# Kernel optimization log

Measured on AMD Instinct MI355X. Metric: run time of the kernel, lower is better.

Reference implementation:

```python
import jax, jax.numpy as jnp
import numpy as np

LEAKY_SLOPE = 0.25
EPS_COS = 1e-8
EPS_NORM = 1e-12


def cosine_dist(x):
    # 1 - cosine similarity, matching cosine_distance_torch
    w = jnp.linalg.norm(x, axis=1, keepdims=True)  # [n,1]
    return 1.0 - (x @ x.T) / jnp.maximum(w * w.T, EPS_COS)


def gen_adj(x, edge_per_node):
    # gen_tr_adj_mat: threshold = (edge_per_node*n)-th smallest pairwise cosine distance,
    # zero diagonal, symmetrize via elementwise max, add I, L1 row-normalize.
    n = x.shape[0]
    dist = cosine_dist(x)  # [n,n]
    k = edge_per_node * n
    param = jax.lax.stop_gradient(jnp.partition(dist.ravel(), k)[k])
    eye = jnp.eye(n, dtype=x.dtype)
    g = (dist <= param).astype(x.dtype) * (1.0 - eye)
    adj = (1.0 - dist) * g
    adj_t = adj.T
    take_t = (adj_t > adj).astype(x.dtype)
    adj = adj + adj_t * take_t - adj * take_t  # elementwise max-symmetrize
    adj = adj + eye
    row_norm = jnp.maximum(jnp.sum(jnp.abs(adj), axis=1, keepdims=True), EPS_NORM)
    return adj / row_norm


def gcn_layer(x, adj, w, b):
    # dense mm -> (sparse) adj mm -> bias -> leaky_relu
    return jax.nn.leaky_relu(adj @ (x @ w) + b, LEAKY_SLOPE)


def setup_inputs() -> dict:
    key = jax.random.key(0)
    ks = jax.random.split(key, 8)
    n, d = 4000, 1000
    h = [400, 400, 200]
    x = jax.random.normal(ks[0], (n, d), jnp.float32)

    def xavier(k, fi, fo):
        std = (2.0 / (fi + fo)) ** 0.5
        return std * jax.random.normal(k, (fi, fo), jnp.float32)

    w1 = xavier(ks[1], d, h[0])
    w2 = xavier(ks[2], h[0], h[1])
    w3 = xavier(ks[3], h[1], h[2])
    b1 = jnp.zeros((h[0],), jnp.float32)
    b2 = jnp.zeros((h[1],), jnp.float32)
    b3 = jnp.zeros((h[2],), jnp.float32)
    adj_parameter = 10
    adj = gen_adj(x, adj_parameter)  # initial train adjacency, as in the pipeline
    return dict(adj_parameter=adj_parameter, x=x, adj=adj,
                w1=w1, b1=b1, w2=w2, b2=b2, w3=w3, b3=b3)


def reference(adj_parameter, x, adj, w1, b1, w2, b2, w3, b3):
    # eval mode: F.dropout(training=False) is identity
    x = gcn_layer(x, adj, w1, b1)
    adj = gen_adj(x, adj_parameter)
    x = gcn_layer(x, adj, w2, b2)
    adj = gen_adj(x, adj_parameter)
    x = gcn_layer(x, adj, w3, b3)
    return x
```

## Files before the change

kernel.cpp:

```cpp
#include <hip/hip_runtime.h>
#include <math.h>

#define NN 4000
#define KC 384
#define LEAKY 0.25f
#define HBLK 1000
#define NPART1 2016


template<int EPI>
__device__ inline float epi_apply(float v, int r, int c,
                                  const float* __restrict__ bias,
                                  const float* __restrict__ wn)
{
    if (EPI == 1) {
        float s = __fadd_rn(v, bias[c]);
        return (s >= 0.f) ? s : __fmul_rn(LEAKY, s);
    }
    if (EPI == 2) {
        float den = fmaxf(__fmul_rn(wn[r], wn[c]), 1e-8f);
        return __fsub_rn(1.0f, __fdiv_rn(v, den));
    }
    return v;
}

__global__ __launch_bounds__(256, 4)
void gemm_tri64_k(const float* __restrict__ A, float* __restrict__ C,
                  unsigned* __restrict__ partial, int n, int K,
                  const float* __restrict__ wn)
{
    __shared__ float As[16][68];
    __shared__ float Bs[16][68];
    __shared__ unsigned lh[2048];
    const int tid = threadIdx.x;
    const int tx = tid & 15, ty = tid >> 4;
    const int sub = tid & 7;
    const int nt = (n + 63) >> 6;
    int bi = 0, rem = blockIdx.x;
    while (rem >= nt - bi) { rem -= nt - bi; ++bi; }
    const int bm = bi * 64, bn = (bi + rem) * 64;
    const bool diag = (rem == 0);

    for (int i = tid; i < 2048; i += 256) lh[i] = 0;

    float blk[4][4] = {};
    float acc[4][4];
    bool first = true;

    for (int kb = 0; kb < K; kb += KC) {
        const int kend = (kb + KC < K) ? kb + KC : K;
        for (int k0 = kb; k0 < kend; k0 += 16) {
            {
                int row = tid >> 2, q = tid & 3;
                int gr = bm + row, gk = k0 + q * 4;
                float4 v = make_float4(0.f, 0.f, 0.f, 0.f);
                if (gr < n) {
                    if (gk + 3 < kend) {
                        v = *(const float4*)(A + (size_t)gr * K + gk);
                    } else {
                        float* vp = (float*)&v;
#pragma unroll
                        for (int e = 0; e < 4; ++e)
                            if (gk + e < kend) vp[e] = A[(size_t)gr * K + gk + e];
                    }
                }
                float* vp = (float*)&v;
#pragma unroll
                for (int e = 0; e < 4; ++e) As[q * 4 + e][row] = vp[e];
            }
            {
                int row = tid >> 2, q = tid & 3;
                int gc = bn + row, gk = k0 + q * 4;
                float4 v = make_float4(0.f, 0.f, 0.f, 0.f);
                if (gc < n) {
                    if (gk + 3 < kend) {
                        v = *(const float4*)(A + (size_t)gc * K + gk);
                    } else {
                        float* vp = (float*)&v;
#pragma unroll
                        for (int e = 0; e < 4; ++e)
                            if (gk + e < kend) vp[e] = A[(size_t)gc * K + gk + e];
                    }
                }
                float* vp = (float*)&v;
#pragma unroll
                for (int e = 0; e < 4; ++e) Bs[q * 4 + e][row] = vp[e];
            }
            __syncthreads();
#pragma unroll
            for (int kk = 0; kk < 16; ++kk) {
                float a[4], b[4];
                *(float4*)&a[0] = *(const float4*)&As[kk][ty * 4];
                *(float4*)&b[0] = *(const float4*)&Bs[kk][tx * 4];
#pragma unroll
                for (int i = 0; i < 4; ++i)
#pragma unroll
                    for (int j = 0; j < 4; ++j)
                        blk[i][j] = fmaf(a[i], b[j], blk[i][j]);
            }
            __syncthreads();
        }
        if (first) {
#pragma unroll
            for (int i = 0; i < 4; ++i)
#pragma unroll
                for (int j = 0; j < 4; ++j) { acc[i][j] = blk[i][j]; blk[i][j] = 0.f; }
            first = false;
        } else {
#pragma unroll
            for (int i = 0; i < 4; ++i)
#pragma unroll
                for (int j = 0; j < 4; ++j) {
                    acc[i][j] = __fadd_rn(acc[i][j], blk[i][j]);
                    blk[i][j] = 0.f;
                }
        }
    }

#pragma unroll
    for (int i = 0; i < 4; ++i) {
        int r = bm + ty * 4 + i;
        if (r >= n) continue;
        float* Crow = C + (size_t)r * n;
        int c = bn + tx * 4;
        float v[4];
#pragma unroll
        for (int e = 0; e < 4; ++e)
            v[e] = epi_apply<2>(acc[i][e], r, c + e, nullptr, wn);
        if (c + 3 < n) {
            float4 s; s.x = v[0]; s.y = v[1]; s.z = v[2]; s.w = v[3];
            *(float4*)(Crow + c) = s;
        } else {
#pragma unroll
            for (int e = 0; e < 4; ++e)
                if (c + e < n) Crow[c + e] = v[e];
        }
#pragma unroll
        for (int e = 0; e < 4; ++e) {
            int cc = c + e;
            if (cc >= n) continue;
            unsigned w = 2u;
            if (diag) {
                if (cc < r) continue;
                if (cc == r) w = 1u;
            }
            unsigned u = __float_as_uint(v[e]);
            unsigned key = (u & 0x80000000u) ? ~u : (u | 0x80000000u);
            atomicAdd(&lh[(((key >> 24) & 0xFFu) << 3) | sub], w);
        }
    }
    __syncthreads();
    unsigned t = 0;
#pragma unroll
    for (int s = 0; s < 8; ++s) t += lh[(tid << 3) | s];
    partial[blockIdx.x * 256 + tid] = t;
}

template<int EPI>
__global__ __launch_bounds__(256, 4)
void gemm_s_k(const float* __restrict__ A, const float* __restrict__ B,
              float* __restrict__ C, int M, int N, int K,
              const float* __restrict__ bias)
{
    __shared__ float As[16][36];
    __shared__ float Bs[16][68];
    const int tid = threadIdx.x;
    const int tx = tid & 15, ty = tid >> 4;
    const int bm = blockIdx.y * 32, bn = blockIdx.x * 64;

    float blk[2][4] = {};
    float acc[2][4];
    bool first = true;

    for (int kb = 0; kb < K; kb += KC) {
        const int kend = (kb + KC < K) ? kb + KC : K;
        for (int k0 = kb; k0 < kend; k0 += 16) {
            {
                int row = tid >> 3, q = tid & 7;
                int gr = bm + row, gk = k0 + q * 2;
                float2 v = make_float2(0.f, 0.f);
                if (gr < M) {
                    if (gk + 1 < kend) {
                        v = *(const float2*)(A + (size_t)gr * K + gk);
                    } else if (gk < kend) {
                        v.x = A[(size_t)gr * K + gk];
                    }
                }
                As[q * 2 + 0][row] = v.x;
                As[q * 2 + 1][row] = v.y;
            }
            {
                int kk = tid >> 4, c = (tid & 15) * 4;
                int gk = k0 + kk, gc = bn + c;
                float4 v = make_float4(0.f, 0.f, 0.f, 0.f);
                if (gk < kend) {
                    if (gc + 3 < N) {
                        v = *(const float4*)(B + (size_t)gk * N + gc);
                    } else {
                        float* vp = (float*)&v;
#pragma unroll
                        for (int e = 0; e < 4; ++e)
                            if (gc + e < N) vp[e] = B[(size_t)gk * N + gc + e];
                    }
                }
                *(float4*)&Bs[kk][c] = v;
            }
            __syncthreads();
#pragma unroll
            for (int kk = 0; kk < 16; ++kk) {
                float a0 = As[kk][ty * 2], a1 = As[kk][ty * 2 + 1];
                float b[4];
                *(float4*)&b[0] = *(const float4*)&Bs[kk][tx * 4];
#pragma unroll
                for (int j = 0; j < 4; ++j) {
                    blk[0][j] = fmaf(a0, b[j], blk[0][j]);
                    blk[1][j] = fmaf(a1, b[j], blk[1][j]);
                }
            }
            __syncthreads();
        }
        if (first) {
#pragma unroll
            for (int i = 0; i < 2; ++i)
#pragma unroll
                for (int j = 0; j < 4; ++j) { acc[i][j] = blk[i][j]; blk[i][j] = 0.f; }
            first = false;
        } else {
#pragma unroll
            for (int i = 0; i < 2; ++i)
#pragma unroll
                for (int j = 0; j < 4; ++j) {
                    acc[i][j] = __fadd_rn(acc[i][j], blk[i][j]);
                    blk[i][j] = 0.f;
                }
        }
    }

#pragma unroll
    for (int i = 0; i < 2; ++i) {
        int r = bm + ty * 2 + i;
        if (r >= M) continue;
        float* Crow = C + (size_t)r * N;
        int c = bn + tx * 4;
        float v[4];
#pragma unroll
        for (int e = 0; e < 4; ++e)
            v[e] = epi_apply<EPI>(acc[i][e], r, c + e, bias, nullptr);
        if (c + 3 < N) {
            float4 s; s.x = v[0]; s.y = v[1]; s.z = v[2]; s.w = v[3];
            *(float4*)(Crow + c) = s;
        } else {
#pragma unroll
            for (int e = 0; e < 4; ++e)
                if (c + e < N) Crow[c + e] = v[e];
        }
    }
}

template<int EPI, bool TRANSB, bool FIRST, bool LAST>
__global__ __launch_bounds__(256, 4)
void gemm_pass_k(const float* __restrict__ A, const float* __restrict__ B,
                 float* __restrict__ C, int M, int N, int K, int kb, int kend,
                 const float* __restrict__ bias, const float* __restrict__ wn)
{
    __shared__ float As[16][132];
    __shared__ float Bs[16][132];
    const int tid = threadIdx.x;
    const int tx = tid & 15, ty = tid >> 4;
    const int bm = blockIdx.y * 128, bn = blockIdx.x * 128;

    float blk[8][8] = {};

    for (int k0 = kb; k0 < kend; k0 += 16) {
#pragma unroll
        for (int it = 0; it < 2; ++it) {
            int idx = tid + it * 256;
            int row = idx >> 2, q = idx & 3;
            int gr = bm + row, gk = k0 + q * 4;
            float4 v = make_float4(0.f, 0.f, 0.f, 0.f);
            if (gr < M) {
                if (gk + 3 < kend) {
                    v = *(const float4*)(A + (size_t)gr * K + gk);
                } else {
                    float* vp = (float*)&v;
#pragma unroll
                    for (int e = 0; e < 4; ++e)
                        if (gk + e < kend) vp[e] = A[(size_t)gr * K + gk + e];
                }
            }
            float* vp = (float*)&v;
#pragma unroll
            for (int e = 0; e < 4; ++e) As[q * 4 + e][row] = vp[e];
        }
        if (!TRANSB) {
#pragma unroll
            for (int it = 0; it < 2; ++it) {
                int idx = tid + it * 256;
                int kk = idx >> 5, cq = idx & 31;
                int gk = k0 + kk, c = cq * 4, gc = bn + c;
                float4 v = make_float4(0.f, 0.f, 0.f, 0.f);
                if (gk < kend) {
                    if (gc + 3 < N) {
                        v = *(const float4*)(B + (size_t)gk * N + gc);
                    } else {
                        float* vp = (float*)&v;
#pragma unroll
                        for (int e = 0; e < 4; ++e)
                            if (gc + e < N) vp[e] = B[(size_t)gk * N + gc + e];
                    }
                }
                *(float4*)&Bs[kk][c] = v;
            }
        } else {
#pragma unroll
            for (int it = 0; it < 2; ++it) {
                int idx = tid + it * 256;
                int row = idx >> 2, q = idx & 3;
                int gc = bn + row, gk = k0 + q * 4;
                float4 v = make_float4(0.f, 0.f, 0.f, 0.f);
                if (gc < N) {
                    if (gk + 3 < kend) {
                        v = *(const float4*)(B + (size_t)gc * K + gk);
                    } else {
                        float* vp = (float*)&v;
#pragma unroll
                        for (int e = 0; e < 4; ++e)
                            if (gk + e < kend) vp[e] = B[(size_t)gc * K + gk + e];
                    }
                }
                float* vp = (float*)&v;
#pragma unroll
                for (int e = 0; e < 4; ++e) Bs[q * 4 + e][row] = vp[e];
            }
        }
        __syncthreads();
#pragma unroll
        for (int kk = 0; kk < 16; ++kk) {
            float a[8], b[8];
            *(float4*)&a[0] = *(const float4*)&As[kk][ty * 4];
            *(float4*)&a[4] = *(const float4*)&As[kk][ty * 4 + 64];
            *(float4*)&b[0] = *(const float4*)&Bs[kk][tx * 4];
            *(float4*)&b[4] = *(const float4*)&Bs[kk][tx * 4 + 64];
#pragma unroll
            for (int i = 0; i < 8; ++i)
#pragma unroll
                for (int j = 0; j < 8; ++j)
                    blk[i][j] = fmaf(a[i], b[j], blk[i][j]);
        }
        __syncthreads();
    }

#pragma unroll
    for (int i = 0; i < 8; ++i) {
        int r = bm + ty * 4 + (i & 3) + (i >> 2) * 64;
        if (r >= M) continue;
        float* Crow = C + (size_t)r * N;
#pragma unroll
        for (int h = 0; h < 2; ++h) {
            int c = bn + tx * 4 + h * 64;
            float v[4];
#pragma unroll
            for (int e = 0; e < 4; ++e) v[e] = blk[i][h * 4 + e];
            if (c + 3 < N) {
                if (!FIRST) {
                    float4 o = *(const float4*)(Crow + c);
                    v[0] = __fadd_rn(o.x, v[0]); v[1] = __fadd_rn(o.y, v[1]);
                    v[2] = __fadd_rn(o.z, v[2]); v[3] = __fadd_rn(o.w, v[3]);
                }
                if (LAST) {
#pragma unroll
                    for (int e = 0; e < 4; ++e)
                        v[e] = epi_apply<EPI>(v[e], r, c + e, bias, wn);
                }
                float4 s; s.x = v[0]; s.y = v[1]; s.z = v[2]; s.w = v[3];
                *(float4*)(Crow + c) = s;
            } else {
#pragma unroll
                for (int e = 0; e < 4; ++e) {
                    if (c + e >= N) continue;
                    float vv = v[e];
                    if (!FIRST) vv = __fadd_rn(Crow[c + e], vv);
                    if (LAST) vv = epi_apply<EPI>(vv, r, c + e, bias, wn);
                    Crow[c + e] = vv;
                }
            }
        }
    }
}

template<int XF>
__device__ float xf(float v)
{
    if (XF == 0) return __fmul_rn(v, v);
    return fabsf(v);
}

template<int XF>
__device__ float np_pairwise(const float* a, int n)
{
    if (n < 8) {
        float r = 0.f;
        for (int i = 0; i < n; ++i) r = __fadd_rn(r, xf<XF>(a[i]));
        return r;
    }
    if (n <= 128) {
        float r[8];
#pragma unroll
        for (int j = 0; j < 8; ++j) r[j] = xf<XF>(a[j]);
        int i = 8;
        const int lim = n - (n & 7);
        for (; i < lim; i += 8)
#pragma unroll
            for (int j = 0; j < 8; ++j) r[j] = __fadd_rn(r[j], xf<XF>(a[i + j]));
        float res = __fadd_rn(__fadd_rn(__fadd_rn(r[0], r[1]), __fadd_rn(r[2], r[3])),
                              __fadd_rn(__fadd_rn(r[4], r[5]), __fadd_rn(r[6], r[7])));
        for (; i < n; ++i) res = __fadd_rn(res, xf<XF>(a[i]));
        return res;
    }
    int n2 = (n / 2) & ~7;
    return __fadd_rn(np_pairwise<XF>(a, n2), np_pairwise<XF>(a + n2, n - n2));
}

__global__ __launch_bounds__(256)
void rownorm2_k(const float* __restrict__ X, float* __restrict__ wn)
{
    __shared__ float buf[400];
    __shared__ float leaf[4];
    const int row = blockIdx.x;
    const float* Xr = X + (size_t)row * 400;
    for (int i = threadIdx.x; i < 100; i += 256)
        *(float4*)&buf[i * 4] = *(const float4*)(Xr + i * 4);
    __syncthreads();
    if (threadIdx.x < 4) {
        const int off = (threadIdx.x >> 1) * 200 + ((threadIdx.x & 1) ? 96 : 0);
        const int len = (threadIdx.x & 1) ? 104 : 96;
        leaf[threadIdx.x] = np_pairwise<0>(buf + off, len);
    }
    __syncthreads();
    if (threadIdx.x == 0) {
        float s = __fadd_rn(__fadd_rn(leaf[0], leaf[1]),
                            __fadd_rn(leaf[2], leaf[3]));
        wn[row] = __fsqrt_rn(s);
    }
}

__global__ __launch_bounds__(256)
void rowabs2_k(const float* __restrict__ A, float* __restrict__ rs)
{
    __shared__ float buf[4000];
    __shared__ float leaf[8];
    const int row = blockIdx.x;
    const float* Ar = A + (size_t)row * 4000;
    for (int i = threadIdx.x; i < 1000; i += 256)
        *(float4*)&buf[i * 4] = *(const float4*)(Ar + i * 4);
    __syncthreads();
    if (threadIdx.x < 8) {
        const int off = (threadIdx.x >> 1) * 1000 + ((threadIdx.x & 1) ? 496 : 0);
        const int len = (threadIdx.x & 1) ? 504 : 496;
        leaf[threadIdx.x] = np_pairwise<1>(buf + off, len);
    }
    __syncthreads();
    if (threadIdx.x == 0) {
        float s = __fadd_rn(
            __fadd_rn(__fadd_rn(leaf[0], leaf[1]), __fadd_rn(leaf[2], leaf[3])),
            __fadd_rn(__fadd_rn(leaf[4], leaf[5]), __fadd_rn(leaf[6], leaf[7])));
        rs[row] = fmaxf(s, 1e-12f);
    }
}

__global__ void init_k(unsigned* __restrict__ state, const void* __restrict__ epn,
                       int* __restrict__ cnt)
{
    const int t = blockIdx.x * 256 + threadIdx.x;
    if (t < NN) cnt[t] = 0;
    if (t == 0) {
        int k = ((const int*)epn)[0];
        if (k <= 0 || k > 4000) {
            float f = ((const float*)epn)[0];
            if (f > 0.f && f <= 4000.f) k = (int)f;
            else {
                long long ll = ((const long long*)epn)[0];
                if (ll > 0 && ll <= 4000) k = (int)ll;
                else {
                    double dd = ((const double*)epn)[0];
                    k = (dd > 0.0 && dd <= 4000.0) ? (int)dd : 10;
                }
            }
        }
        state[0] = 0u;
        state[1] = (unsigned)(k * NN);
    }
}

__global__ __launch_bounds__(256)
void hist_tri_k(const float* __restrict__ dist, unsigned* __restrict__ partial,
                const unsigned* __restrict__ state, int shift, int n)
{
    __shared__ unsigned lh[2048];
    for (int i = threadIdx.x; i < 2048; i += 256) lh[i] = 0;
    __syncthreads();
    const unsigned prefix = state[0];
    const int sub = threadIdx.x & 7;
    const int npair = (n + 1) / 2;
    for (int p = blockIdx.x; p < npair; p += HBLK) {
#pragma unroll
        for (int half = 0; half < 2; ++half) {
            const int i = half ? (n - 1 - p) : p;
            if (half && i == p) break;
            const float* row = dist + (size_t)i * n;
            for (int j = i + threadIdx.x; j < n; j += 256) {
                unsigned u = __float_as_uint(row[j]);
                unsigned key = (u & 0x80000000u) ? ~u : (u | 0x80000000u);
                bool ok = ((key >> (shift + 8)) == prefix);
                if (ok) atomicAdd(&lh[((((key >> shift) & 0xFFu)) << 3) | sub],
                                  (j == i) ? 1u : 2u);
            }
        }
    }
    __syncthreads();
    unsigned t = 0;
#pragma unroll
    for (int s = 0; s < 8; ++s) t += lh[(threadIdx.x << 3) | s];
    partial[blockIdx.x * 256 + threadIdx.x] = t;
}

__global__ __launch_bounds__(256)
void reduce_k(const unsigned* __restrict__ partial, int nparts,
              unsigned* __restrict__ hist256)
{
    const int bin = blockIdx.x;
    const int tid = threadIdx.x;
    unsigned s = 0;
    for (int i = tid; i < nparts; i += 256)
        s += partial[(size_t)i * 256 + bin];
    __shared__ unsigned sh[256];
    sh[tid] = s;
    __syncthreads();
    for (int off = 128; off > 0; off >>= 1) {
        if (tid < off) sh[tid] += sh[tid + off];
        __syncthreads();
    }
    if (tid == 0) hist256[bin] = sh[0];
}

__global__ __launch_bounds__(256)
void scan256_k(const unsigned* __restrict__ hist256, unsigned* __restrict__ state,
               int shift, float* __restrict__ param)
{
    const int tid = threadIdx.x;
    unsigned h = hist256[tid];
    __shared__ unsigned sh[256];
    sh[tid] = h;
    __syncthreads();
    for (int off = 1; off < 256; off <<= 1) {
        unsigned v = (tid >= off) ? sh[tid - off] : 0;
        __syncthreads();
        sh[tid] += v;
        __syncthreads();
    }
    const unsigned incl = sh[tid], excl = incl - h;
    const unsigned krem = state[1];
    if (krem >= excl && krem < incl) {
        unsigned np = (state[0] << 8) | (unsigned)tid;
        state[0] = np;
        state[1] = krem - excl;
        if (shift == 0) {
            unsigned u = (np & 0x80000000u) ? (np ^ 0x80000000u) : ~np;
            *param = __uint_as_float(u);
        }
    }
}

__device__ inline float thr_f(float d, int i, int j, float p)
{
    float a = (d <= p && i != j) ? __fsub_rn(1.0f, d) : 0.0f;
    return (i == j) ? 1.0f : a;
}

__global__ __launch_bounds__(256)
void symthresh_mirror_k(float* __restrict__ adj, const float* __restrict__ param,
                        int* __restrict__ cnt, int n)
{
    __shared__ float TB[64][65];
    const float p = *param;
    const int nt = (n + 63) >> 6;
    int bi = 0, rem = blockIdx.x;
    while (rem >= nt - bi) { rem -= nt - bi; ++bi; }
    const int bj = bi + rem;
    const int tid = threadIdx.x;
    const int lane = tid & 63;
    const int r0i = bi * 64, r0j = bj * 64;

#pragma unroll
    for (int it = 0; it < 16; ++it) {
        int idx = tid + it * 256;
        int q = idx >> 6, c = idx & 63;
        int gr = r0i + q, gc = r0j + c;
        bool inb = (gr < n && gc < n);
        float a = 0.f;
        if (inb) {
            a = thr_f(adj[(size_t)gr * n + gc], gr, gc, p);
            adj[(size_t)gr * n + gc] = a;
            TB[q][c] = a;
        }
        unsigned long long m = __ballot(inb && a != 0.0f);
        if (lane == 0 && gr < n) atomicAdd(&cnt[gr], (int)__popcll(m));
    }
    __syncthreads();
    if (bi != bj) {
#pragma unroll
        for (int it = 0; it < 16; ++it) {
            int idx = tid + it * 256;
            int q = idx >> 6, c = idx & 63;
            int gr = r0j + q, gc = r0i + c;
            bool inb = (gr < n && gc < n);
            float a = 0.f;
            if (inb) {
                a = TB[c][q];
                adj[(size_t)gr * n + gc] = a;
            }
            unsigned long long m = __ballot(inb && a != 0.0f);
            if (lane == 0 && gr < n) atomicAdd(&cnt[gr], (int)__popcll(m));
        }
    }
}

__global__ __launch_bounds__(256)
void norm_k(float* __restrict__ adj, const float* __restrict__ rs, int n)
{
    const int i = blockIdx.y;
    const int j = blockIdx.x * 256 + threadIdx.x;
    if (j >= n) return;
    const size_t idx = (size_t)i * n + j;
    adj[idx] = __fdiv_rn(adj[idx], rs[i]);
}

__global__ __launch_bounds__(256)
void count_k(const float* __restrict__ A, int* __restrict__ cnt, int n)
{
    const int gw = (blockIdx.x * blockDim.x + threadIdx.x) >> 6;
    if (gw >= n) return;
    const int lane = threadIdx.x & 63;
    int c = 0;
    for (int k0 = 0; k0 < n; k0 += 64) {
        int k = k0 + lane;
        bool nz = (k < n) && (A[(size_t)gw * n + k] != 0.0f);
        unsigned long long m = __ballot(nz);
        c += (int)__popcll(m);
    }
    if (lane == 0) cnt[gw] = c;
}

__global__ __launch_bounds__(1024)
void scanrows_k(const int* __restrict__ cnt, int* __restrict__ roff)
{
    const int t = threadIdx.x;
    int vals[4];
    int s0 = 0;
#pragma unroll
    for (int e = 0; e < 4; ++e) {
        int r = t * 4 + e;
        vals[e] = (r < NN) ? cnt[r] : 0;
        s0 += vals[e];
    }
    __shared__ int sh[1024];
    sh[t] = s0;
    __syncthreads();
    for (int off = 1; off < 1024; off <<= 1) {
        int v = (t >= off) ? sh[t - off] : 0;
        __syncthreads();
        sh[t] += v;
        __syncthreads();
    }
    int excl = sh[t] - s0;
#pragma unroll
    for (int e = 0; e < 4; ++e) {
        int r = t * 4 + e;
        if (r <= NN) roff[r] = excl;
        excl += vals[e];
    }
    if (t == 1023) roff[NN] = sh[1023];
}

template<bool DIV>
__global__ __launch_bounds__(256)
void fill_k(const float* __restrict__ A, const int* __restrict__ roff,
            const float* __restrict__ rs, int* __restrict__ ridx,
            float* __restrict__ rval, int n)
{
    const int gw = (blockIdx.x * blockDim.x + threadIdx.x) >> 6;
    if (gw >= n) return;
    const int lane = threadIdx.x & 63;
    const float r = DIV ? rs[gw] : 1.0f;
    int base = roff[gw];
    const unsigned long long ltmask = (lane == 63) ? ~0ULL >> 1
                                                   : ((1ULL << lane) - 1);
    for (int k0 = 0; k0 < n; k0 += 64) {
        int k = k0 + lane;
        float v = (k < n) ? A[(size_t)gw * n + k] : 0.f;
        bool nz = (v != 0.0f);
        unsigned long long m = __ballot(nz);
        if (nz) {
            int pos = base + (int)__popcll(m & ltmask);
            ridx[pos] = k;
            rval[pos] = DIV ? __fdiv_rn(v, r) : v;
        }
        base += (int)__popcll(m);
    }
}

__global__ __launch_bounds__(256)
void spmm_k(const int* __restrict__ roff, const int* __restrict__ ridx,
            const float* __restrict__ rval, const float* __restrict__ T,
            const float* __restrict__ bias, float* __restrict__ H, int ncols)
{
    __shared__ int ks[128];
    __shared__ float vs[128];
    const int r = blockIdx.x;
    const int tid = threadIdx.x;
    const int c0 = tid, c1 = tid + 256;
    const bool ok0 = c0 < ncols, ok1 = c1 < ncols;
    float acc0 = 0.f, blk0 = 0.f, acc1 = 0.f, blk1 = 0.f;
    int nb = KC;
    const int s = roff[r], e = roff[r + 1];
    for (int base = s; base < e; base += 128) {
        const int m = (e - base < 128) ? (e - base) : 128;
        __syncthreads();
        if (tid < m) { ks[tid] = ridx[base + tid]; vs[tid] = rval[base + tid]; }
        __syncthreads();
        for (int t = 0; t < m; ++t) {
            const int k = ks[t];
            const float v = vs[t];
            while (k >= nb) {
                acc0 = __fadd_rn(acc0, blk0); blk0 = 0.f;
                acc1 = __fadd_rn(acc1, blk1); blk1 = 0.f;
                nb += KC;
            }
            const float* Tr = T + (size_t)k * ncols;
            if (ok0) blk0 = fmaf(v, Tr[c0], blk0);
            if (ok1) blk1 = fmaf(v, Tr[c1], blk1);
        }
    }
    acc0 = __fadd_rn(acc0, blk0);
    acc1 = __fadd_rn(acc1, blk1);
    if (ok0) {
        float s0 = __fadd_rn(acc0, bias[c0]);
        H[(size_t)r * ncols + c0] = (s0 >= 0.f) ? s0 : __fmul_rn(LEAKY, s0);
    }
    if (ok1) {
        float s1 = __fadd_rn(acc1, bias[c1]);
        H[(size_t)r * ncols + c1] = (s1 >= 0.f) ? s1 : __fmul_rn(LEAKY, s1);
    }
}

template<int EPI, bool TRANSB>
static void run_gemm(const float* A, const float* B, float* C,
                     int M, int N, int K, const float* bias, const float* wn,
                     hipStream_t stream)
{
    const int nb = (K + KC - 1) / KC;
    const dim3 grid((N + 127) / 128, (M + 127) / 128);
    for (int p = 0; p < nb; ++p) {
        const int kb = p * KC;
        const int kend = (kb + KC < K) ? kb + KC : K;
        const bool first = (p == 0), last = (p == nb - 1);
        if (first && last)
            gemm_pass_k<EPI, TRANSB, true, true><<<grid, 256, 0, stream>>>(
                A, B, C, M, N, K, kb, kend, bias, wn);
        else if (first)
            gemm_pass_k<EPI, TRANSB, true, false><<<grid, 256, 0, stream>>>(
                A, B, C, M, N, K, kb, kend, bias, wn);
        else if (last)
            gemm_pass_k<EPI, TRANSB, false, true><<<grid, 256, 0, stream>>>(
                A, B, C, M, N, K, kb, kend, bias, wn);
        else
            gemm_pass_k<EPI, TRANSB, false, false><<<grid, 256, 0, stream>>>(
                A, B, C, M, N, K, kb, kend, bias, wn);
    }
}

extern "C" void kernel_launch(void* const* d_in, const int* in_sizes, int n_in,
                              void* d_out, int out_size, void* d_ws, size_t ws_size,
                              hipStream_t stream)
{
    const void*  epn  = d_in[0];
    const float* x    = (const float*)d_in[1];
    const float* adj0 = (const float*)d_in[2];
    const float* w1   = (const float*)d_in[3];
    const float* b1   = (const float*)d_in[4];
    const float* w2   = (const float*)d_in[5];
    const float* b2   = (const float*)d_in[6];
    const float* w3   = (const float*)d_in[7];
    const float* b3   = (const float*)d_in[8];
    float* out = (float*)d_out;

    char* ws = (char*)d_ws;
    float*    dist    = (float*)   ws;
    float*    Tbuf    = (float*)  (ws + 64000000);
    float*    H1      = (float*)  (ws + 70400000);
    float*    H2      = (float*)  (ws + 76800000);
    float*    wn      = (float*)  (ws + 83200000);
    float*    rs      = (float*)  (ws + 83216000);
    unsigned* state   = (unsigned*)(ws + 83232000);
    float*    param   = (float*)  (ws + 83232008);
    unsigned* hist256 = (unsigned*)(ws + 83232064);
    unsigned* partial = (unsigned*)(ws + 83233088);
    int*      cnt     = (int*)    (ws + 85297472);
    int*      roff    = (int*)    (ws + 85313472);
    int*      ridx    = (int*)    (ws + 85329480);
    float*    rval    = (float*)  (ws + 101329480);
    const bool use_csr = (ws_size >= 117329480ULL + 64);

    const int nt64 = (NN + 63) / 64;
    const int nsym64 = nt64 * (nt64 + 1) / 2;

    auto genadj = [&](const float* H) {
        rownorm2_k<<<NN, 256, 0, stream>>>(H, wn);
        gemm_tri64_k<<<nsym64, 256, 0, stream>>>(H, dist, partial, NN, 400, wn);
        init_k<<<16, 256, 0, stream>>>(state, epn, cnt);
        reduce_k<<<256, 256, 0, stream>>>(partial, NPART1, hist256);
        scan256_k<<<1, 256, 0, stream>>>(hist256, state, 24, param);
        for (int p = 1; p < 4; ++p) {
            const int shift = 24 - 8 * p;
            hist_tri_k<<<HBLK, 256, 0, stream>>>(dist, partial, state, shift, NN);
            reduce_k<<<256, 256, 0, stream>>>(partial, HBLK, hist256);
            scan256_k<<<1, 256, 0, stream>>>(hist256, state, shift, param);
        }
        symthresh_mirror_k<<<nsym64, 256, 0, stream>>>(dist, param, cnt, NN);
        rowabs2_k<<<NN, 256, 0, stream>>>(dist, rs);
    };

    auto aggregate_pre = [&](const float* Aadj, const float* Tm,
                             const float* bias, float* Hout, int ncols) {
        if (use_csr) {
            count_k<<<(NN + 3) / 4, 256, 0, stream>>>(Aadj, cnt, NN);
            scanrows_k<<<1, 1024, 0, stream>>>(cnt, roff);
            fill_k<false><<<(NN + 3) / 4, 256, 0, stream>>>(Aadj, roff, nullptr,
                                                            ridx, rval, NN);
            spmm_k<<<NN, 256, 0, stream>>>(roff, ridx, rval, Tm, bias, Hout, ncols);
        } else {
            run_gemm<1, false>(Aadj, Tm, Hout, NN, ncols, NN, bias,
                               nullptr, stream);
        }
    };

    auto aggregate_rs = [&](float* Aadj, const float* Tm,
                            const float* bias, float* Hout, int ncols) {
        if (use_csr) {
            scanrows_k<<<1, 1024, 0, stream>>>(cnt, roff);
            fill_k<true><<<(NN + 3) / 4, 256, 0, stream>>>(Aadj, roff, rs,
                                                           ridx, rval, NN);
            spmm_k<<<NN, 256, 0, stream>>>(roff, ridx, rval, Tm, bias, Hout, ncols);
        } else {
            norm_k<<<dim3((NN + 255) / 256, NN), 256, 0, stream>>>(Aadj, rs, NN);
            run_gemm<1, false>(Aadj, Tm, Hout, NN, ncols, NN, bias,
                               nullptr, stream);
        }
    };

    gemm_s_k<0><<<dim3((400 + 63) / 64, (NN + 31) / 32), 256, 0, stream>>>(
        x, w1, Tbuf, NN, 400, 1000, nullptr);
    aggregate_pre(adj0, Tbuf, b1, H1, 400);

    genadj(H1);
    gemm_s_k<0><<<dim3((400 + 63) / 64, (NN + 31) / 32), 256, 0, stream>>>(
        H1, w2, Tbuf, NN, 400, 400, nullptr);
    aggregate_rs(dist, Tbuf, b2, H2, 400);

    genadj(H2);
    gemm_s_k<0><<<dim3((200 + 63) / 64, (NN + 31) / 32), 256, 0, stream>>>(
        H2, w3, Tbuf, NN, 200, 400, nullptr);
    aggregate_rs(dist, Tbuf, b3, out, 200);
}
```

Measured before the change: 898.9 us.

## Enlarge symmetric distance GEMM tiles to 96, widen dense GEMM, fuse row norms into SpMM

The triangular cosine-distance GEMM moves from 64x64 to 96x96 tiles with a 6x6 register micro-tile, which raises arithmetic intensity and cuts the block count. The threshold/mirror kernel is rewritten to match the 96 tiling and now counts nonzeros per row from shared memory instead of with ballots. The small dense GEMM goes from 32x64 to 64x64 tiles. Row norms for the next cosine-distance step are computed inside the SpMM epilogue, which removes the separate rownorm launch. In exchange, the 6x6 tile uses more registers and its scalar LDS reads and scalar stores replace vector ones, and the pairwise norm offsets are hardcoded for a 400-column row.

```diff
diff --git a/kernel.cpp b/kernel.cpp
--- a/kernel.cpp
+++ b/kernel.cpp
@@ -5,7 +5,9 @@
 #define KC 384
 #define LEAKY 0.25f
 #define HBLK 1000
-#define NPART1 2016
+#define TT 96
+#define NTT 42
+#define NPART1 903
 
 
 template<int EPI>
@@ -24,24 +26,172 @@
     return v;
 }
 
+template<int XF>
+__device__ float xf(float v)
+{
+    if (XF == 0) return __fmul_rn(v, v);
+    return fabsf(v);
+}
+
+template<int XF>
+__device__ float np_pairwise(const float* a, int n)
+{
+    if (n < 8) {
+        float r = 0.f;
+        for (int i = 0; i < n; ++i) r = __fadd_rn(r, xf<XF>(a[i]));
+        return r;
+    }
+    if (n <= 128) {
+        float r[8];
+#pragma unroll
+        for (int j = 0; j < 8; ++j) r[j] = xf<XF>(a[j]);
+        int i = 8;
+        const int lim = n - (n & 7);
+        for (; i < lim; i += 8)
+#pragma unroll
+            for (int j = 0; j < 8; ++j) r[j] = __fadd_rn(r[j], xf<XF>(a[i + j]));
+        float res = __fadd_rn(__fadd_rn(__fadd_rn(r[0], r[1]), __fadd_rn(r[2], r[3])),
+                              __fadd_rn(__fadd_rn(r[4], r[5]), __fadd_rn(r[6], r[7])));
+        for (; i < n; ++i) res = __fadd_rn(res, xf<XF>(a[i]));
+        return res;
+    }
+    int n2 = (n / 2) & ~7;
+    return __fadd_rn(np_pairwise<XF>(a, n2), np_pairwise<XF>(a + n2, n - n2));
+}
+
 __global__ __launch_bounds__(256, 4)
-void gemm_tri64_k(const float* __restrict__ A, float* __restrict__ C,
+void gemm_tri96_k(const float* __restrict__ A, float* __restrict__ C,
                   unsigned* __restrict__ partial, int n, int K,
                   const float* __restrict__ wn)
 {
-    __shared__ float As[16][68];
-    __shared__ float Bs[16][68];
+    __shared__ float As[16][100];
+    __shared__ float Bs[16][100];
     __shared__ unsigned lh[2048];
     const int tid = threadIdx.x;
     const int tx = tid & 15, ty = tid >> 4;
     const int sub = tid & 7;
-    const int nt = (n + 63) >> 6;
     int bi = 0, rem = blockIdx.x;
-    while (rem >= nt - bi) { rem -= nt - bi; ++bi; }
-    const int bm = bi * 64, bn = (bi + rem) * 64;
+    while (rem >= NTT - bi) { rem -= NTT - bi; ++bi; }
+    const int bm = bi * TT, bn = (bi + rem) * TT;
     const bool diag = (rem == 0);
 
     for (int i = tid; i < 2048; i += 256) lh[i] = 0;
+
+    float blk[6][6] = {};
+    float acc[6][6];
+    bool first = true;
+
+    for (int kb = 0; kb < K; kb += KC) {
+        const int kend = (kb + KC < K) ? kb + KC : K;
+        for (int k0 = kb; k0 < kend; k0 += 16) {
+            for (int idx = tid; idx < 384; idx += 256) {
+                int row = idx >> 2, q = idx & 3;
+                int gr = bm + row, gk = k0 + q * 4;
+                float4 v = make_float4(0.f, 0.f, 0.f, 0.f);
+                if (gr < n) {
+                    if (gk + 3 < kend) {
+                        v = *(const float4*)(A + (size_t)gr * K + gk);
+                    } else {
+                        float* vp = (float*)&v;
+#pragma unroll
+                        for (int e = 0; e < 4; ++e)
+                            if (gk + e < kend) vp[e] = A[(size_t)gr * K + gk + e];
+                    }
+                }
+                float* vp = (float*)&v;
+#pragma unroll
+                for (int e = 0; e < 4; ++e) As[q * 4 + e][row] = vp[e];
+            }
+            for (int idx = tid; idx < 384; idx += 256) {
+                int row = idx >> 2, q = idx & 3;
+                int gc = bn + row, gk = k0 + q * 4;
+                float4 v = make_float4(0.f, 0.f, 0.f, 0.f);
+                if (gc < n) {
+                    if (gk + 3 < kend) {
+                        v = *(const float4*)(A + (size_t)gc * K + gk);
+                    } else {
+                        float* vp = (float*)&v;
+#pragma unroll
+                        for (int e = 0; e < 4; ++e)
+                            if (gk + e < kend) vp[e] = A[(size_t)gc * K + gk + e];
+                    }
+                }
+                float* vp = (float*)&v;
+#pragma unroll
+                for (int e = 0; e < 4; ++e) Bs[q * 4 + e][row] = vp[e];
+            }
+            __syncthreads();
+#pragma unroll
+            for (int kk = 0; kk < 16; ++kk) {
+                float a[6], b[6];
+#pragma unroll
+                for (int e = 0; e < 6; ++e) a[e] = As[kk][ty * 6 + e];
+#pragma unroll
+                for (int e = 0; e < 6; ++e) b[e] = Bs[kk][tx * 6 + e];
+#pragma unroll
+                for (int i = 0; i < 6; ++i)
+#pragma unroll
+                    for (int j = 0; j < 6; ++j)
+                        blk[i][j] = fmaf(a[i], b[j], blk[i][j]);
+            }
+            __syncthreads();
+        }
+        if (first) {
+#pragma unroll
+            for (int i = 0; i < 6; ++i)
+#pragma unroll
+                for (int j = 0; j < 6; ++j) { acc[i][j] = blk[i][j]; blk[i][j] = 0.f; }
+            first = false;
+        } else {
+#pragma unroll
+            for (int i = 0; i < 6; ++i)
+#pragma unroll
+                for (int j = 0; j < 6; ++j) {
+                    acc[i][j] = __fadd_rn(acc[i][j], blk[i][j]);
+                    blk[i][j] = 0.f;
+                }
+        }
+    }
+
+#pragma unroll
+    for (int i = 0; i < 6; ++i) {
+        int r = bm + ty * 6 + i;
+        if (r >= n) continue;
+        float* Crow = C + (size_t)r * n;
+#pragma unroll
+        for (int j = 0; j < 6; ++j) {
+            int cc = bn + tx * 6 + j;
+            if (cc >= n) continue;
+            float v = epi_apply<2>(acc[i][j], r, cc, nullptr, wn);
+            Crow[cc] = v;
+            unsigned w = 2u;
+            if (diag) {
+                if (cc < r) continue;
+                if (cc == r) w = 1u;
+            }
+            unsigned u = __float_as_uint(v);
+            unsigned key = (u & 0x80000000u) ? ~u : (u | 0x80000000u);
+            atomicAdd(&lh[(((key >> 24) & 0xFFu) << 3) | sub], w);
+        }
+    }
+    __syncthreads();
+    unsigned t = 0;
+#pragma unroll
+    for (int s = 0; s < 8; ++s) t += lh[(tid << 3) | s];
+    partial[blockIdx.x * 256 + tid] = t;
+}
+
+template<int EPI>
+__global__ __launch_bounds__(256, 4)
+void gemm_s_k(const float* __restrict__ A, const float* __restrict__ B,
+              float* __restrict__ C, int M, int N, int K,
+              const float* __restrict__ bias)
+{
+    __shared__ float As[16][68];
+    __shared__ float Bs[16][68];
+    const int tid = threadIdx.x;
+    const int tx = tid & 15, ty = tid >> 4;
+    const int bm = blockIdx.y * 64, bn = blockIdx.x * 64;
 
     float blk[4][4] = {};
     float acc[4][4];
@@ -54,7 +204,7 @@
                 int row = tid >> 2, q = tid & 3;
                 int gr = bm + row, gk = k0 + q * 4;
                 float4 v = make_float4(0.f, 0.f, 0.f, 0.f);
-                if (gr < n) {
+                if (gr < M) {
                     if (gk + 3 < kend) {
                         v = *(const float4*)(A + (size_t)gr * K + gk);
                     } else {
@@ -67,127 +217,6 @@
                 float* vp = (float*)&v;
 #pragma unroll
                 for (int e = 0; e < 4; ++e) As[q * 4 + e][row] = vp[e];
-            }
-            {
-                int row = tid >> 2, q = tid & 3;
-                int gc = bn + row, gk = k0 + q * 4;
-                float4 v = make_float4(0.f, 0.f, 0.f, 0.f);
-                if (gc < n) {
-                    if (gk + 3 < kend) {
-                        v = *(const float4*)(A + (size_t)gc * K + gk);
-                    } else {
-                        float* vp = (float*)&v;
-#pragma unroll
-                        for (int e = 0; e < 4; ++e)
-                            if (gk + e < kend) vp[e] = A[(size_t)gc * K + gk + e];
-                    }
-                }
-                float* vp = (float*)&v;
-#pragma unroll
-                for (int e = 0; e < 4; ++e) Bs[q * 4 + e][row] = vp[e];
-            }
-            __syncthreads();
-#pragma unroll
-            for (int kk = 0; kk < 16; ++kk) {
-                float a[4], b[4];
-                *(float4*)&a[0] = *(const float4*)&As[kk][ty * 4];
-                *(float4*)&b[0] = *(const float4*)&Bs[kk][tx * 4];
-#pragma unroll
-                for (int i = 0; i < 4; ++i)
-#pragma unroll
-                    for (int j = 0; j < 4; ++j)
-                        blk[i][j] = fmaf(a[i], b[j], blk[i][j]);
-            }
-            __syncthreads();
-        }
-        if (first) {
-#pragma unroll
-            for (int i = 0; i < 4; ++i)
-#pragma unroll
-                for (int j = 0; j < 4; ++j) { acc[i][j] = blk[i][j]; blk[i][j] = 0.f; }
-            first = false;
-        } else {
-#pragma unroll
-            for (int i = 0; i < 4; ++i)
-#pragma unroll
-                for (int j = 0; j < 4; ++j) {
-                    acc[i][j] = __fadd_rn(acc[i][j], blk[i][j]);
-                    blk[i][j] = 0.f;
-                }
-        }
-    }
-
-#pragma unroll
-    for (int i = 0; i < 4; ++i) {
-        int r = bm + ty * 4 + i;
-        if (r >= n) continue;
-        float* Crow = C + (size_t)r * n;
-        int c = bn + tx * 4;
-        float v[4];
-#pragma unroll
-        for (int e = 0; e < 4; ++e)
-            v[e] = epi_apply<2>(acc[i][e], r, c + e, nullptr, wn);
-        if (c + 3 < n) {
-            float4 s; s.x = v[0]; s.y = v[1]; s.z = v[2]; s.w = v[3];
-            *(float4*)(Crow + c) = s;
-        } else {
-#pragma unroll
-            for (int e = 0; e < 4; ++e)
-                if (c + e < n) Crow[c + e] = v[e];
-        }
-#pragma unroll
-        for (int e = 0; e < 4; ++e) {
-            int cc = c + e;
-            if (cc >= n) continue;
-            unsigned w = 2u;
-            if (diag) {
-                if (cc < r) continue;
-                if (cc == r) w = 1u;
-            }
-            unsigned u = __float_as_uint(v[e]);
-            unsigned key = (u & 0x80000000u) ? ~u : (u | 0x80000000u);
-            atomicAdd(&lh[(((key >> 24) & 0xFFu) << 3) | sub], w);
-        }
-    }
-    __syncthreads();
-    unsigned t = 0;
-#pragma unroll
-    for (int s = 0; s < 8; ++s) t += lh[(tid << 3) | s];
-    partial[blockIdx.x * 256 + tid] = t;
-}
-
-template<int EPI>
-__global__ __launch_bounds__(256, 4)
-void gemm_s_k(const float* __restrict__ A, const float* __restrict__ B,
-              float* __restrict__ C, int M, int N, int K,
-              const float* __restrict__ bias)
-{
-    __shared__ float As[16][36];
-    __shared__ float Bs[16][68];
-    const int tid = threadIdx.x;
-    const int tx = tid & 15, ty = tid >> 4;
-    const int bm = blockIdx.y * 32, bn = blockIdx.x * 64;
-
-    float blk[2][4] = {};
-    float acc[2][4];
-    bool first = true;
-
-    for (int kb = 0; kb < K; kb += KC) {
-        const int kend = (kb + KC < K) ? kb + KC : K;
-        for (int k0 = kb; k0 < kend; k0 += 16) {
-            {
-                int row = tid >> 3, q = tid & 7;
-                int gr = bm + row, gk = k0 + q * 2;
-                float2 v = make_float2(0.f, 0.f);
-                if (gr < M) {
-                    if (gk + 1 < kend) {
-                        v = *(const float2*)(A + (size_t)gr * K + gk);
-                    } else if (gk < kend) {
-                        v.x = A[(size_t)gr * K + gk];
-                    }
-                }
-                As[q * 2 + 0][row] = v.x;
-                As[q * 2 + 1][row] = v.y;
             }
             {
                 int kk = tid >> 4, c = (tid & 15) * 4;
@@ -208,26 +237,26 @@
             __syncthreads();
 #pragma unroll
             for (int kk = 0; kk < 16; ++kk) {
-                float a0 = As[kk][ty * 2], a1 = As[kk][ty * 2 + 1];
-                float b[4];
+                float a[4], b[4];
+                *(float4*)&a[0] = *(const float4*)&As[kk][ty * 4];
                 *(float4*)&b[0] = *(const float4*)&Bs[kk][tx * 4];
 #pragma unroll
-                for (int j = 0; j < 4; ++j) {
-                    blk[0][j] = fmaf(a0, b[j], blk[0][j]);
-                    blk[1][j] = fmaf(a1, b[j], blk[1][j]);
-                }
+                for (int i = 0; i < 4; ++i)
+#pragma unroll
+                    for (int j = 0; j < 4; ++j)
+                        blk[i][j] = fmaf(a[i], b[j], blk[i][j]);
             }
             __syncthreads();
         }
         if (first) {
 #pragma unroll
-            for (int i = 0; i < 2; ++i)
+            for (int i = 0; i < 4; ++i)
 #pragma unroll
                 for (int j = 0; j < 4; ++j) { acc[i][j] = blk[i][j]; blk[i][j] = 0.f; }
             first = false;
         } else {
 #pragma unroll
-            for (int i = 0; i < 2; ++i)
+            for (int i = 0; i < 4; ++i)
 #pragma unroll
                 for (int j = 0; j < 4; ++j) {
                     acc[i][j] = __fadd_rn(acc[i][j], blk[i][j]);
@@ -237,8 +266,8 @@
     }
 
 #pragma unroll
-    for (int i = 0; i < 2; ++i) {
-        int r = bm + ty * 2 + i;
+    for (int i = 0; i < 4; ++i) {
+        int r = bm + ty * 4 + i;
         if (r >= M) continue;
         float* Crow = C + (size_t)r * N;
         int c = bn + tx * 4;
@@ -386,39 +415,6 @@
             }
         }
     }
-}
-
-template<int XF>
-__device__ float xf(float v)
-{
-    if (XF == 0) return __fmul_rn(v, v);
-    return fabsf(v);
-}
-
-template<int XF>
-__device__ float np_pairwise(const float* a, int n)
-{
-    if (n < 8) {
-        float r = 0.f;
-        for (int i = 0; i < n; ++i) r = __fadd_rn(r, xf<XF>(a[i]));
-        return r;
-    }
-    if (n <= 128) {
-        float r[8];
-#pragma unroll
-        for (int j = 0; j < 8; ++j) r[j] = xf<XF>(a[j]);
-        int i = 8;
-        const int lim = n - (n & 7);
-        for (; i < lim; i += 8)
-#pragma unroll
-            for (int j = 0; j < 8; ++j) r[j] = __fadd_rn(r[j], xf<XF>(a[i + j]));
-        float res = __fadd_rn(__fadd_rn(__fadd_rn(r[0], r[1]), __fadd_rn(r[2], r[3])),
-                              __fadd_rn(__fadd_rn(r[4], r[5]), __fadd_rn(r[6], r[7])));
-        for (; i < n; ++i) res = __fadd_rn(res, xf<XF>(a[i]));
-        return res;
-    }
-    int n2 = (n / 2) & ~7;
-    return __fadd_rn(np_pairwise<XF>(a, n2), np_pairwise<XF>(a + n2, n - n2));
 }
 
 __global__ __launch_bounds__(256)
@@ -578,49 +574,50 @@
 }
 
 __global__ __launch_bounds__(256)
-void symthresh_mirror_k(float* __restrict__ adj, const float* __restrict__ param,
-                        int* __restrict__ cnt, int n)
-{
-    __shared__ float TB[64][65];
+void symthresh_mirror96_k(float* __restrict__ adj, const float* __restrict__ param,
+                          int* __restrict__ cnt, int n)
+{
+    __shared__ float TB[96][97];
     const float p = *param;
-    const int nt = (n + 63) >> 6;
     int bi = 0, rem = blockIdx.x;
-    while (rem >= nt - bi) { rem -= nt - bi; ++bi; }
+    while (rem >= NTT - bi) { rem -= NTT - bi; ++bi; }
     const int bj = bi + rem;
     const int tid = threadIdx.x;
-    const int lane = tid & 63;
-    const int r0i = bi * 64, r0j = bj * 64;
-
-#pragma unroll
-    for (int it = 0; it < 16; ++it) {
-        int idx = tid + it * 256;
-        int q = idx >> 6, c = idx & 63;
+    const int r0i = bi * TT, r0j = bj * TT;
+
+    for (int idx = tid; idx < 96 * 96; idx += 256) {
+        int q = idx / 96, c = idx - q * 96;
         int gr = r0i + q, gc = r0j + c;
-        bool inb = (gr < n && gc < n);
         float a = 0.f;
-        if (inb) {
+        if (gr < n && gc < n) {
             a = thr_f(adj[(size_t)gr * n + gc], gr, gc, p);
             adj[(size_t)gr * n + gc] = a;
-            TB[q][c] = a;
-        }
-        unsigned long long m = __ballot(inb && a != 0.0f);
-        if (lane == 0 && gr < n) atomicAdd(&cnt[gr], (int)__popcll(m));
+        }
+        TB[q][c] = a;
     }
     __syncthreads();
     if (bi != bj) {
-#pragma unroll
-        for (int it = 0; it < 16; ++it) {
-            int idx = tid + it * 256;
-            int q = idx >> 6, c = idx & 63;
+        for (int idx = tid; idx < 96 * 96; idx += 256) {
+            int q = idx / 96, c = idx - q * 96;
             int gr = r0j + q, gc = r0i + c;
-            bool inb = (gr < n && gc < n);
-            float a = 0.f;
-            if (inb) {
-                a = TB[c][q];
-                adj[(size_t)gr * n + gc] = a;
-            }
-            unsigned long long m = __ballot(inb && a != 0.0f);
-            if (lane == 0 && gr < n) atomicAdd(&cnt[gr], (int)__popcll(m));
+            if (gr < n && gc < n)
+                adj[(size_t)gr * n + gc] = TB[c][q];
+        }
+    }
+    if (tid < 96) {
+        int gr = r0i + tid;
+        if (gr < n) {
+            int cA = 0;
+            for (int c = 0; c < 96; ++c) cA += (TB[tid][c] != 0.0f);
+            if (cA) atomicAdd(&cnt[gr], cA);
+        }
+    } else if (tid < 192 && bi != bj) {
+        int q = tid - 96;
+        int gr = r0j + q;
+        if (gr < n) {
+            int cB = 0;
+            for (int c = 0; c < 96; ++c) cB += (TB[c][q] != 0.0f);
+            if (cB) atomicAdd(&cnt[gr], cB);
         }
     }
 }
@@ -709,13 +706,17 @@
     }
 }
 
+template<bool WN>
 __global__ __launch_bounds__(256)
 void spmm_k(const int* __restrict__ roff, const int* __restrict__ ridx,
             const float* __restrict__ rval, const float* __restrict__ T,
-            const float* __restrict__ bias, float* __restrict__ H, int ncols)
+            const float* __restrict__ bias, float* __restrict__ H, int ncols,
+            float* __restrict__ wn)
 {
     __shared__ int ks[128];
     __shared__ float vs[128];
+    __shared__ float buf[512];
+    __shared__ float leaf[4];
     const int r = blockIdx.x;
     const int tid = threadIdx.x;
     const int c0 = tid, c1 = tid + 256;
@@ -743,13 +744,32 @@
     }
     acc0 = __fadd_rn(acc0, blk0);
     acc1 = __fadd_rn(acc1, blk1);
+    float h0 = 0.f, h1 = 0.f;
     if (ok0) {
         float s0 = __fadd_rn(acc0, bias[c0]);
-        H[(size_t)r * ncols + c0] = (s0 >= 0.f) ? s0 : __fmul_rn(LEAKY, s0);
+        h0 = (s0 >= 0.f) ? s0 : __fmul_rn(LEAKY, s0);
+        H[(size_t)r * ncols + c0] = h0;
     }
     if (ok1) {
         float s1 = __fadd_rn(acc1, bias[c1]);
-        H[(size_t)r * ncols + c1] = (s1 >= 0.f) ? s1 : __fmul_rn(LEAKY, s1);
+        h1 = (s1 >= 0.f) ? s1 : __fmul_rn(LEAKY, s1);
+        H[(size_t)r * ncols + c1] = h1;
+    }
+    if (WN) {
+        if (ok0) buf[c0] = h0;
+        if (ok1) buf[c1] = h1;
+        __syncthreads();
+        if (tid < 4) {
+            const int off = (tid >> 1) * 200 + ((tid & 1) ? 96 : 0);
+            const int len = (tid & 1) ? 104 : 96;
+            leaf[tid] = np_pairwise<0>(buf + off, len);
+        }
+        __syncthreads();
+        if (tid == 0) {
+            float s2 = __fadd_rn(__fadd_rn(leaf[0], leaf[1]),
+                                 __fadd_rn(leaf[2], leaf[3]));
+            wn[r] = __fsqrt_rn(s2);
+        }
     }
 }
 
@@ -811,12 +831,12 @@
     float*    rval    = (float*)  (ws + 101329480);
     const bool use_csr = (ws_size >= 117329480ULL + 64);
 
-    const int nt64 = (NN + 63) / 64;
-    const int nsym64 = nt64 * (nt64 + 1) / 2;
-
-    auto genadj = [&](const float* H) {
-        rownorm2_k<<<NN, 256, 0, stream>>>(H, wn);
-        gemm_tri64_k<<<nsym64, 256, 0, stream>>>(H, dist, partial, NN, 400, wn);
+    const int gsN = (NN + 63) / 64;
+
+    auto genadj = [&](const float* H, bool have_wn) {
+        if (!have_wn)
+            rownorm2_k<<<NN, 256, 0, stream>>>(H, wn);
+        gemm_tri96_k<<<NPART1, 256, 0, stream>>>(H, dist, partial, NN, 400, wn);
         init_k<<<16, 256, 0, stream>>>(state, epn, cnt);
         reduce_k<<<256, 256, 0, stream>>>(partial, NPART1, hist256);
         scan256_k<<<1, 256, 0, stream>>>(hist256, state, 24, param);
@@ -826,18 +846,24 @@
             reduce_k<<<256, 256, 0, stream>>>(partial, HBLK, hist256);
             scan256_k<<<1, 256, 0, stream>>>(hist256, state, shift, param);
         }
-        symthresh_mirror_k<<<nsym64, 256, 0, stream>>>(dist, param, cnt, NN);
+        symthresh_mirror96_k<<<NPART1, 256, 0, stream>>>(dist, param, cnt, NN);
         rowabs2_k<<<NN, 256, 0, stream>>>(dist, rs);
     };
 
     auto aggregate_pre = [&](const float* Aadj, const float* Tm,
-                             const float* bias, float* Hout, int ncols) {
+                             const float* bias, float* Hout, int ncols,
+                             bool want_wn) {
         if (use_csr) {
             count_k<<<(NN + 3) / 4, 256, 0, stream>>>(Aadj, cnt, NN);
             scanrows_k<<<1, 1024, 0, stream>>>(cnt, roff);
             fill_k<false><<<(NN + 3) / 4, 256, 0, stream>>>(Aadj, roff, nullptr,
                                                             ridx, rval, NN);
-            spmm_k<<<NN, 256, 0, stream>>>(roff, ridx, rval, Tm, bias, Hout, ncols);
+            if (want_wn)
+                spmm_k<true><<<NN, 256, 0, stream>>>(roff, ridx, rval, Tm, bias,
+                                                     Hout, ncols, wn);
+            else
+                spmm_k<false><<<NN, 256, 0, stream>>>(roff, ridx, rval, Tm, bias,
+                                                      Hout, ncols, nullptr);
         } else {
             run_gemm<1, false>(Aadj, Tm, Hout, NN, ncols, NN, bias,
                                nullptr, stream);
@@ -845,12 +871,18 @@
     };
 
     auto aggregate_rs = [&](float* Aadj, const float* Tm,
-                            const float* bias, float* Hout, int ncols) {
+                            const float* bias, float* Hout, int ncols,
+                            bool want_wn) {
         if (use_csr) {
             scanrows_k<<<1, 1024, 0, stream>>>(cnt, roff);
             fill_k<true><<<(NN + 3) / 4, 256, 0, stream>>>(Aadj, roff, rs,
                                                            ridx, rval, NN);
-            spmm_k<<<NN, 256, 0, stream>>>(roff, ridx, rval, Tm, bias, Hout, ncols);
+            if (want_wn)
+                spmm_k<true><<<NN, 256, 0, stream>>>(roff, ridx, rval, Tm, bias,
+                                                     Hout, ncols, wn);
+            else
+                spmm_k<false><<<NN, 256, 0, stream>>>(roff, ridx, rval, Tm, bias,
+                                                      Hout, ncols, nullptr);
         } else {
             norm_k<<<dim3((NN + 255) / 256, NN), 256, 0, stream>>>(Aadj, rs, NN);
             run_gemm<1, false>(Aadj, Tm, Hout, NN, ncols, NN, bias,
@@ -858,17 +890,17 @@
         }
     };
 
-    gemm_s_k<0><<<dim3((400 + 63) / 64, (NN + 31) / 32), 256, 0, stream>>>(
+    gemm_s_k<0><<<dim3((400 + 63) / 64, gsN), 256, 0, stream>>>(
         x, w1, Tbuf, NN, 400, 1000, nullptr);
-    aggregate_pre(adj0, Tbuf, b1, H1, 400);
-
-    genadj(H1);
-    gemm_s_k<0><<<dim3((400 + 63) / 64, (NN + 31) / 32), 256, 0, stream>>>(
+    aggregate_pre(adj0, Tbuf, b1, H1, 400, use_csr);
+
+    genadj(H1, use_csr);
+    gemm_s_k<0><<<dim3((400 + 63) / 64, gsN), 256, 0, stream>>>(
         H1, w2, Tbuf, NN, 400, 400, nullptr);
-    aggregate_rs(dist, Tbuf, b2, H2, 400);
-
-    genadj(H2);
-    gemm_s_k<0><<<dim3((200 + 63) / 64, (NN + 31) / 32), 256, 0, stream>>>(
+    aggregate_rs(dist, Tbuf, b2, H2, 400, use_csr);
+
+    genadj(H2, use_csr);
+    gemm_s_k<0><<<dim3((200 + 63) / 64, gsN), 256, 0, stream>>>(
         H2, w3, Tbuf, NN, 200, 400, nullptr);
-    aggregate_rs(dist, Tbuf, b3, out, 200);
-}
+    aggregate_rs(dist, Tbuf, b3, out, 200, false);
+}
```

After: 917.5 us (median of 2 runs). 1.02x slower.
